# Kernel optimization log

Hardware: AMD Instinct MI355X
Metric: run time of the kernel (lower is better)

## Reference

```python
import jax, jax.numpy as jnp
import numpy as np

N, D = 16384, 128
T = 0.07


def setup_inputs() -> dict:
    key = jax.random.key(0)
    k1, k2 = jax.random.split(key)
    anchors = jax.random.normal(k1, (N, D), dtype=jnp.float32)
    positives = jax.random.normal(k2, (N, D), dtype=jnp.float32)
    return {"anchors": anchors, "positives": positives}


def reference(anchors, positives):
    # L2-normalize along feature dim (eps matches torch F.normalize default 1e-12)
    a = anchors / jnp.maximum(jnp.linalg.norm(anchors, axis=-1, keepdims=True), 1e-12)
    p = positives / jnp.maximum(jnp.linalg.norm(positives, axis=-1, keepdims=True), 1e-12)
    logits = (a @ p.T) / T  # [N, N]
    # cross-entropy with diagonal labels, mean reduction
    logz = jax.nn.logsumexp(logits, axis=-1)  # [N]
    diag = jnp.diagonal(logits)  # [N]
    return jnp.mean(logz - diag)
```

## Files before the change

### kernel.cpp

```cpp
#include <hip/hip_runtime.h>
#include <hip/hip_bf16.h>

#define N_ROWS 16384
#define DIM 128

constexpr float INV_T = 1.0f / 0.07f;
constexpr float LOG2E = 1.4426950408889634f;
constexpr float C1    = INV_T * LOG2E;
constexpr float SOP   = 4.5398160f;
constexpr float LN2   = 0.69314718055994530942f;

typedef int   v4i    __attribute__((ext_vector_type(4)));
typedef int   v8i    __attribute__((ext_vector_type(8)));
typedef float f32x16 __attribute__((ext_vector_type(16)));

typedef const __attribute__((address_space(1))) void* gptr1_t;
typedef __attribute__((address_space(3))) void*       sptr3_t;

#define TILE_BYTES 4096
#define BM 256
#define WROWS 64
#define COLSPLIT 16
#define COLS_PER (N_ROWS / COLSPLIT)
#define NJT (COLS_PER / 32)

__global__ __launch_bounds__(256) void norm_kernel(
    const float* __restrict__ A, const float* __restrict__ P,
    ushort* __restrict__ a8u, ushort* __restrict__ p8u,
    float* __restrict__ diag, float* __restrict__ sacc)
{
    if (threadIdx.x < 4) sacc[blockIdx.x * 4 + threadIdx.x] = 0.f;
    int row  = blockIdx.x * 4 + (threadIdx.x >> 6);
    int lane = threadIdx.x & 63;
    float2 av = *(const float2*)(A + (size_t)row * DIM + lane * 2);
    float2 pv = *(const float2*)(P + (size_t)row * DIM + lane * 2);
    float ssa = av.x * av.x + av.y * av.y;
    float ssp = pv.x * pv.x + pv.y * pv.y;
    float dp  = av.x * pv.x + av.y * pv.y;
    #pragma unroll
    for (int m = 1; m < 64; m <<= 1) {
        ssa += __shfl_xor(ssa, m);
        ssp += __shfl_xor(ssp, m);
        dp  += __shfl_xor(dp,  m);
    }
    float ra = 1.0f / fmaxf(sqrtf(ssa), 1e-12f);
    float rp = 1.0f / fmaxf(sqrtf(ssp), 1e-12f);
    if (lane == 0) diag[row] = dp * ra * rp * INV_T;
    float sa = ra * SOP, sp = rp * SOP;
    int apk = __builtin_amdgcn_cvt_pk_fp8_f32(av.x * sa, av.y * sa, 0, false);
    int ppk = __builtin_amdgcn_cvt_pk_fp8_f32(pv.x * sp, pv.y * sp, 0, false);
    a8u[(size_t)row * 64 + lane] = (ushort)apk;
    size_t off = (size_t)(row >> 5) * 2048 + (lane >> 5) * 1024
               + ((lane >> 4) & 1) * 512 + ((lane >> 3) & 1) * 256
               + (row & 31) * 8 + (lane & 7);
    p8u[off] = (ushort)ppk;
}

__global__ __launch_bounds__(256, 2) void lse_kernel(
    const ushort* __restrict__ a8u, const ushort* __restrict__ p8u,
    float* __restrict__ s_accum)
{
    __shared__ __attribute__((aligned(16))) char btile[3][TILE_BYTES];

    int colseg = blockIdx.x & (COLSPLIT - 1);
    int rowblk = blockIdx.x / COLSPLIT;
    int wave = threadIdx.x >> 6;
    int lane = threadIdx.x & 63;
    int c31  = lane & 31, hi = lane >> 5;
    int row0 = rowblk * BM + wave * WROWS;

    const char* a8 = (const char*)a8u;
    v8i afA0 = *(const v8i*)(a8 + (size_t)(row0 + c31) * 128 +       hi * 32);
    v8i afA1 = *(const v8i*)(a8 + (size_t)(row0 + c31) * 128 + 64  + hi * 32);
    v8i afB0 = *(const v8i*)(a8 + (size_t)(row0 + 32 + c31) * 128 +      hi * 32);
    v8i afB1 = *(const v8i*)(a8 + (size_t)(row0 + 32 + c31) * 128 + 64 + hi * 32);

    f32x16 cinit;
    #pragma unroll
    for (int r = 0; r < 16; ++r) cinit[r] = -C1;

    float s0[16], s1[16];
    #pragma unroll
    for (int r = 0; r < 16; ++r) { s0[r] = 0.f; s1[r] = 0.f; }

    const char* seg = (const char*)p8u + (size_t)colseg * NJT * TILE_BYTES;
    char* lds = (char*)&btile[0][0];
    int choff = wave * 1024 + lane * 16;

    auto STAGE = [&](int t, int buf) {
        __builtin_amdgcn_global_load_lds(
            (gptr1_t)(seg + (size_t)t * TILE_BYTES + choff),
            (sptr3_t)(lds + buf * TILE_BYTES + choff), 16, 0, 0);
    };

    int rdoff = hi * 1024 + c31 * 16;

    f32x16 acc0, acc1;

    STAGE(0, 0);
    STAGE(1, 1);

    for (int jt = 0; jt < NJT; ++jt) {
        if (jt < NJT - 1) asm volatile("s_waitcnt vmcnt(1)" ::: "memory");
        else              asm volatile("s_waitcnt vmcnt(0)" ::: "memory");
        __builtin_amdgcn_s_barrier();
        __builtin_amdgcn_sched_barrier(0);

        if (jt + 2 < NJT) STAGE(jt + 2, (jt + 2) % 3);

        const char* tb = lds + (jt % 3) * TILE_BYTES;
        v4i x0 = *(const v4i*)(tb + rdoff);
        v4i y0 = *(const v4i*)(tb + rdoff + 512);
        v4i x1 = *(const v4i*)(tb + 2048 + rdoff);
        v4i y1 = *(const v4i*)(tb + 2048 + rdoff + 512);
        v8i b0, b1;
        #pragma unroll
        for (int j = 0; j < 4; ++j) {
            b0[j] = x0[j]; b0[4 + j] = y0[j];
            b1[j] = x1[j]; b1[4 + j] = y1[j];
        }

        __builtin_amdgcn_s_setprio(1);
        acc0 = __builtin_amdgcn_mfma_scale_f32_32x32x64_f8f6f4(
            afA0, b0, cinit, 0, 0, 0, 0x7f7f7f7f, 0, 0x7f7f7f7f);
        acc1 = __builtin_amdgcn_mfma_scale_f32_32x32x64_f8f6f4(
            afB0, b0, cinit, 0, 0, 0, 0x7f7f7f7f, 0, 0x7f7f7f7f);
        acc0 = __builtin_amdgcn_mfma_scale_f32_32x32x64_f8f6f4(
            afA1, b1, acc0, 0, 0, 0, 0x7f7f7f7f, 0, 0x7f7f7f7f);
        acc1 = __builtin_amdgcn_mfma_scale_f32_32x32x64_f8f6f4(
            afB1, b1, acc1, 0, 0, 0, 0x7f7f7f7f, 0, 0x7f7f7f7f);
        __builtin_amdgcn_s_setprio(0);

        #pragma unroll
        for (int r = 0; r < 16; ++r) {
            s0[r] += __builtin_amdgcn_exp2f(acc0[r]);
            s1[r] += __builtin_amdgcn_exp2f(acc1[r]);
        }
    }

    #pragma unroll
    for (int t = 0; t < 2; ++t)
        #pragma unroll
        for (int r = 0; r < 16; ++r) {
            float v = (t ? s1[r] : s0[r]);
            v += __shfl_xor(v, 1);
            v += __shfl_xor(v, 2);
            v += __shfl_xor(v, 4);
            v += __shfl_xor(v, 8);
            v += __shfl_xor(v, 16);
            if (c31 == 0)
                atomicAdd(&s_accum[row0 + t * 32 + (r & 3) + 8 * (r >> 2) + 4 * hi], v);
        }
}

__global__ __launch_bounds__(1024) void finalize_kernel(
    const float* __restrict__ s_acc, const float* __restrict__ diag,
    float* __restrict__ out)
{
    float acc = 0.f;
    int t = threadIdx.x;
    #pragma unroll
    for (int i = 0; i < 4; ++i) {
        int idx = (i * 1024 + t) * 4;
        float4 sv = *(const float4*)(s_acc + idx);
        float4 dv = *(const float4*)(diag + idx);
        acc += __builtin_amdgcn_logf(sv.x) * LN2 + INV_T - dv.x;
        acc += __builtin_amdgcn_logf(sv.y) * LN2 + INV_T - dv.y;
        acc += __builtin_amdgcn_logf(sv.z) * LN2 + INV_T - dv.z;
        acc += __builtin_amdgcn_logf(sv.w) * LN2 + INV_T - dv.w;
    }
    #pragma unroll
    for (int m = 1; m < 64; m <<= 1) acc += __shfl_xor(acc, m);
    __shared__ float wsum[16];
    if ((t & 63) == 0) wsum[t >> 6] = acc;
    __syncthreads();
    if (t == 0) {
        float r = 0.f;
        #pragma unroll
        for (int i = 0; i < 16; ++i) r += wsum[i];
        out[0] = r / (float)N_ROWS;
    }
}

extern "C" void kernel_launch(void* const* d_in, const int* in_sizes, int n_in,
                              void* d_out, int out_size, void* d_ws, size_t ws_size,
                              hipStream_t stream)
{
    const float* A = (const float*)d_in[0];
    const float* P = (const float*)d_in[1];
    float* out = (float*)d_out;

    char* ws = (char*)d_ws;
    ushort* a8u  = (ushort*)ws;
    ushort* p8u  = (ushort*)(ws + (size_t)2 * 1024 * 1024);
    float*  diag = (float*)(ws + (size_t)4 * 1024 * 1024);
    float*  sacc = (float*)(ws + (size_t)4 * 1024 * 1024 + 65536);

    norm_kernel<<<N_ROWS / 4, 256, 0, stream>>>(A, P, a8u, p8u, diag, sacc);
    lse_kernel<<<(N_ROWS / BM) * COLSPLIT, 256, 0, stream>>>(a8u, p8u, sacc);
    finalize_kernel<<<1, 1024, 0, stream>>>(sacc, diag, out);
}
```

Before: 62.85 us.

## Use single-wave blocks with private double-buffered B tiles, dropping barriers

The LSE kernel moves from 256-thread blocks, where four waves share a triple-buffered B tile, to 64-thread single-wave blocks. Each wave now stages the whole 4KB tile itself with four global_load_lds calls into a double buffer. The next prefetch is issued only after the LDS reads finish (lgkmcnt(0)), so no s_barrier is needed. This removes the cross-wave barrier stalls, but each B tile is now fetched four times as often from global/L2 and blocks are smaller, which changes occupancy and scheduling.

```diff
diff --git a/kernel.cpp b/kernel.cpp
--- a/kernel.cpp
+++ b/kernel.cpp
@@ -18,7 +18,6 @@
 typedef __attribute__((address_space(3))) void*       sptr3_t;
 
 #define TILE_BYTES 4096
-#define BM 256
 #define WROWS 64
 #define COLSPLIT 16
 #define COLS_PER (N_ROWS / COLSPLIT)
@@ -56,18 +55,17 @@
     p8u[off] = (ushort)ppk;
 }
 
-__global__ __launch_bounds__(256, 2) void lse_kernel(
+__global__ __launch_bounds__(64) void lse_kernel(
     const ushort* __restrict__ a8u, const ushort* __restrict__ p8u,
     float* __restrict__ s_accum)
 {
-    __shared__ __attribute__((aligned(16))) char btile[3][TILE_BYTES];
+    __shared__ __attribute__((aligned(16))) char btile[2][TILE_BYTES];
 
     int colseg = blockIdx.x & (COLSPLIT - 1);
-    int rowblk = blockIdx.x / COLSPLIT;
-    int wave = threadIdx.x >> 6;
-    int lane = threadIdx.x & 63;
+    int rowwav = blockIdx.x >> 4;
+    int lane = threadIdx.x;
     int c31  = lane & 31, hi = lane >> 5;
-    int row0 = rowblk * BM + wave * WROWS;
+    int row0 = rowwav * WROWS;
 
     const char* a8 = (const char*)a8u;
     v8i afA0 = *(const v8i*)(a8 + (size_t)(row0 + c31) * 128 +       hi * 32);
@@ -85,30 +83,27 @@
 
     const char* seg = (const char*)p8u + (size_t)colseg * NJT * TILE_BYTES;
     char* lds = (char*)&btile[0][0];
-    int choff = wave * 1024 + lane * 16;
+    int loff = lane * 16;
 
     auto STAGE = [&](int t, int buf) {
-        __builtin_amdgcn_global_load_lds(
-            (gptr1_t)(seg + (size_t)t * TILE_BYTES + choff),
-            (sptr3_t)(lds + buf * TILE_BYTES + choff), 16, 0, 0);
+        const char* src = seg + (size_t)t * TILE_BYTES + loff;
+        char* dst = lds + buf * TILE_BYTES + loff;
+        #pragma unroll
+        for (int i = 0; i < 4; ++i)
+            __builtin_amdgcn_global_load_lds(
+                (gptr1_t)(src + i * 1024), (sptr3_t)(dst + i * 1024), 16, 0, 0);
     };
 
     int rdoff = hi * 1024 + c31 * 16;
-
-    f32x16 acc0, acc1;
 
     STAGE(0, 0);
     STAGE(1, 1);
 
     for (int jt = 0; jt < NJT; ++jt) {
-        if (jt < NJT - 1) asm volatile("s_waitcnt vmcnt(1)" ::: "memory");
+        if (jt < NJT - 1) asm volatile("s_waitcnt vmcnt(4)" ::: "memory");
         else              asm volatile("s_waitcnt vmcnt(0)" ::: "memory");
-        __builtin_amdgcn_s_barrier();
-        __builtin_amdgcn_sched_barrier(0);
-
-        if (jt + 2 < NJT) STAGE(jt + 2, (jt + 2) % 3);
-
-        const char* tb = lds + (jt % 3) * TILE_BYTES;
+
+        const char* tb = lds + (jt & 1) * TILE_BYTES;
         v4i x0 = *(const v4i*)(tb + rdoff);
         v4i y0 = *(const v4i*)(tb + rdoff + 512);
         v4i x1 = *(const v4i*)(tb + 2048 + rdoff);
@@ -119,11 +114,15 @@
             b0[j] = x0[j]; b0[4 + j] = y0[j];
             b1[j] = x1[j]; b1[4 + j] = y1[j];
         }
+        asm volatile("s_waitcnt lgkmcnt(0)" ::: "memory");
+        __builtin_amdgcn_sched_barrier(0);
+
+        if (jt + 2 < NJT) STAGE(jt + 2, jt & 1);
 
         __builtin_amdgcn_s_setprio(1);
-        acc0 = __builtin_amdgcn_mfma_scale_f32_32x32x64_f8f6f4(
+        f32x16 acc0 = __builtin_amdgcn_mfma_scale_f32_32x32x64_f8f6f4(
             afA0, b0, cinit, 0, 0, 0, 0x7f7f7f7f, 0, 0x7f7f7f7f);
-        acc1 = __builtin_amdgcn_mfma_scale_f32_32x32x64_f8f6f4(
+        f32x16 acc1 = __builtin_amdgcn_mfma_scale_f32_32x32x64_f8f6f4(
             afB0, b0, cinit, 0, 0, 0, 0x7f7f7f7f, 0, 0x7f7f7f7f);
         acc0 = __builtin_amdgcn_mfma_scale_f32_32x32x64_f8f6f4(
             afA1, b1, acc0, 0, 0, 0, 0x7f7f7f7f, 0, 0x7f7f7f7f);
@@ -197,6 +196,6 @@
     float*  sacc = (float*)(ws + (size_t)4 * 1024 * 1024 + 65536);
 
     norm_kernel<<<N_ROWS / 4, 256, 0, stream>>>(A, P, a8u, p8u, diag, sacc);
-    lse_kernel<<<(N_ROWS / BM) * COLSPLIT, 256, 0, stream>>>(a8u, p8u, sacc);
+    lse_kernel<<<(N_ROWS / WROWS) * COLSPLIT, 64, 0, stream>>>(a8u, p8u, sacc);
     finalize_kernel<<<1, 1024, 0, stream>>>(sacc, diag, out);
 }
```

After: 70.71 us. 1.12x slower.

## Load B tiles directly into registers with double-buffered prefetch, dropping LDS staging

Applied to the files above, without the earlier changes.

Replaces the global_load_lds triple-buffered LDS staging and per-iteration workgroup barriers with direct global-to-register loads of the B fragments. Each wave double-buffers two tiles in registers (even/odd sets) and prefetches the next tile while running MFMA and exp2 on the current one. This removes the barrier and LDS round-trip cost per tile. In exchange, each wave fetches the B tile itself from L2/global instead of sharing one LDS copy across the block, so global traffic per block goes up and more VGPRs are needed.

```diff
diff --git a/kernel.cpp b/kernel.cpp
--- a/kernel.cpp
+++ b/kernel.cpp
@@ -13,9 +13,6 @@
 typedef int   v4i    __attribute__((ext_vector_type(4)));
 typedef int   v8i    __attribute__((ext_vector_type(8)));
 typedef float f32x16 __attribute__((ext_vector_type(16)));
-
-typedef const __attribute__((address_space(1))) void* gptr1_t;
-typedef __attribute__((address_space(3))) void*       sptr3_t;
 
 #define TILE_BYTES 4096
 #define BM 256
@@ -60,8 +57,6 @@
     const ushort* __restrict__ a8u, const ushort* __restrict__ p8u,
     float* __restrict__ s_accum)
 {
-    __shared__ __attribute__((aligned(16))) char btile[3][TILE_BYTES];
-
     int colseg = blockIdx.x & (COLSPLIT - 1);
     int rowblk = blockIdx.x / COLSPLIT;
     int wave = threadIdx.x >> 6;
@@ -83,60 +78,55 @@
     #pragma unroll
     for (int r = 0; r < 16; ++r) { s0[r] = 0.f; s1[r] = 0.f; }
 
-    const char* seg = (const char*)p8u + (size_t)colseg * NJT * TILE_BYTES;
-    char* lds = (char*)&btile[0][0];
-    int choff = wave * 1024 + lane * 16;
+    const char* base = (const char*)p8u
+                     + (size_t)colseg * NJT * TILE_BYTES + hi * 1024 + c31 * 16;
 
-    auto STAGE = [&](int t, int buf) {
-        __builtin_amdgcn_global_load_lds(
-            (gptr1_t)(seg + (size_t)t * TILE_BYTES + choff),
-            (sptr3_t)(lds + buf * TILE_BYTES + choff), 16, 0, 0);
-    };
+    v4i eX0, eY0, eX1, eY1;
+    v4i oX0, oY0, oX1, oY1;
 
-    int rdoff = hi * 1024 + c31 * 16;
+#define LOADSET_E(t) { const char* tb = base + (size_t)(t) * TILE_BYTES;      \
+        eX0 = *(const v4i*)(tb);        eY0 = *(const v4i*)(tb + 512);        \
+        eX1 = *(const v4i*)(tb + 2048); eY1 = *(const v4i*)(tb + 2560); }
+#define LOADSET_O(t) { const char* tb = base + (size_t)(t) * TILE_BYTES;      \
+        oX0 = *(const v4i*)(tb);        oY0 = *(const v4i*)(tb + 512);        \
+        oX1 = *(const v4i*)(tb + 2048); oY1 = *(const v4i*)(tb + 2560); }
 
-    f32x16 acc0, acc1;
+#define COMPUTE(X0, Y0, X1, Y1) {                                             \
+        v8i b0 = __builtin_shufflevector(X0, Y0, 0, 1, 2, 3, 4, 5, 6, 7);     \
+        v8i b1 = __builtin_shufflevector(X1, Y1, 0, 1, 2, 3, 4, 5, 6, 7);     \
+        __builtin_amdgcn_s_setprio(1);                                        \
+        f32x16 acc0 = __builtin_amdgcn_mfma_scale_f32_32x32x64_f8f6f4(        \
+            afA0, b0, cinit, 0, 0, 0, 0x7f7f7f7f, 0, 0x7f7f7f7f);             \
+        f32x16 acc1 = __builtin_amdgcn_mfma_scale_f32_32x32x64_f8f6f4(        \
+            afB0, b0, cinit, 0, 0, 0, 0x7f7f7f7f, 0, 0x7f7f7f7f);             \
+        acc0 = __builtin_amdgcn_mfma_scale_f32_32x32x64_f8f6f4(               \
+            afA1, b1, acc0, 0, 0, 0, 0x7f7f7f7f, 0, 0x7f7f7f7f);              \
+        acc1 = __builtin_amdgcn_mfma_scale_f32_32x32x64_f8f6f4(               \
+            afB1, b1, acc1, 0, 0, 0, 0x7f7f7f7f, 0, 0x7f7f7f7f);              \
+        __builtin_amdgcn_s_setprio(0);                                        \
+        _Pragma("unroll")                                                     \
+        for (int r = 0; r < 16; ++r) {                                        \
+            s0[r] += __builtin_amdgcn_exp2f(acc0[r]);                         \
+            s1[r] += __builtin_amdgcn_exp2f(acc1[r]);                         \
+        } }
 
-    STAGE(0, 0);
-    STAGE(1, 1);
+    LOADSET_E(0);
+    LOADSET_O(1);
 
-    for (int jt = 0; jt < NJT; ++jt) {
-        if (jt < NJT - 1) asm volatile("s_waitcnt vmcnt(1)" ::: "memory");
-        else              asm volatile("s_waitcnt vmcnt(0)" ::: "memory");
-        __builtin_amdgcn_s_barrier();
-        __builtin_amdgcn_sched_barrier(0);
+    for (int m = 0; m < 15; ++m) {
+        v4i x0 = eX0, y0 = eY0, x1 = eX1, y1 = eY1;
+        LOADSET_E(2 * m + 2);
+        COMPUTE(x0, y0, x1, y1);
+        v4i u0 = oX0, v0 = oY0, u1 = oX1, v1 = oY1;
+        LOADSET_O(2 * m + 3);
+        COMPUTE(u0, v0, u1, v1);
+    }
+    COMPUTE(eX0, eY0, eX1, eY1);
+    COMPUTE(oX0, oY0, oX1, oY1);
 
-        if (jt + 2 < NJT) STAGE(jt + 2, (jt + 2) % 3);
-
-        const char* tb = lds + (jt % 3) * TILE_BYTES;
-        v4i x0 = *(const v4i*)(tb + rdoff);
-        v4i y0 = *(const v4i*)(tb + rdoff + 512);
-        v4i x1 = *(const v4i*)(tb + 2048 + rdoff);
-        v4i y1 = *(const v4i*)(tb + 2048 + rdoff + 512);
-        v8i b0, b1;
-        #pragma unroll
-        for (int j = 0; j < 4; ++j) {
-            b0[j] = x0[j]; b0[4 + j] = y0[j];
-            b1[j] = x1[j]; b1[4 + j] = y1[j];
-        }
-
-        __builtin_amdgcn_s_setprio(1);
-        acc0 = __builtin_amdgcn_mfma_scale_f32_32x32x64_f8f6f4(
-            afA0, b0, cinit, 0, 0, 0, 0x7f7f7f7f, 0, 0x7f7f7f7f);
-        acc1 = __builtin_amdgcn_mfma_scale_f32_32x32x64_f8f6f4(
-            afB0, b0, cinit, 0, 0, 0, 0x7f7f7f7f, 0, 0x7f7f7f7f);
-        acc0 = __builtin_amdgcn_mfma_scale_f32_32x32x64_f8f6f4(
-            afA1, b1, acc0, 0, 0, 0, 0x7f7f7f7f, 0, 0x7f7f7f7f);
-        acc1 = __builtin_amdgcn_mfma_scale_f32_32x32x64_f8f6f4(
-            afB1, b1, acc1, 0, 0, 0, 0x7f7f7f7f, 0, 0x7f7f7f7f);
-        __builtin_amdgcn_s_setprio(0);
-
-        #pragma unroll
-        for (int r = 0; r < 16; ++r) {
-            s0[r] += __builtin_amdgcn_exp2f(acc0[r]);
-            s1[r] += __builtin_amdgcn_exp2f(acc1[r]);
-        }
-    }
+#undef LOADSET_E
+#undef LOADSET_O
+#undef COMPUTE
 
     #pragma unroll
     for (int t = 0; t < 2; ++t)
```

Measured after the change: 63.77 us. About the same (+1.5%).

## Halve rows per wave in LSE kernel to one 32-row MFMA tile

Applied to the files above, without the earlier changes.

Each wave now handles 32 anchor rows instead of 64, so the block tile drops from 256 to 128 rows and the grid doubles. Every B tile staged into LDS is therefore used by half as many MFMAs, which doubles the total B traffic and the global-to-LDS staging. In exchange each wave holds fewer registers and more waves can be resident. The exp2 work per wave halves, which may help the exp-bound loop hide latency, but per-block load overhead and atomic count per row stay the same while block count grows.

```diff
diff --git a/kernel.cpp b/kernel.cpp
--- a/kernel.cpp
+++ b/kernel.cpp
@@ -18,8 +18,8 @@
 typedef __attribute__((address_space(3))) void*       sptr3_t;
 
 #define TILE_BYTES 4096
-#define BM 256
-#define WROWS 64
+#define BM 128
+#define WROWS 32
 #define COLSPLIT 16
 #define COLS_PER (N_ROWS / COLSPLIT)
 #define NJT (COLS_PER / 32)
@@ -70,18 +70,12 @@
     int row0 = rowblk * BM + wave * WROWS;
 
     const char* a8 = (const char*)a8u;
-    v8i afA0 = *(const v8i*)(a8 + (size_t)(row0 + c31) * 128 +       hi * 32);
-    v8i afA1 = *(const v8i*)(a8 + (size_t)(row0 + c31) * 128 + 64  + hi * 32);
-    v8i afB0 = *(const v8i*)(a8 + (size_t)(row0 + 32 + c31) * 128 +      hi * 32);
-    v8i afB1 = *(const v8i*)(a8 + (size_t)(row0 + 32 + c31) * 128 + 64 + hi * 32);
+    v8i afA0 = *(const v8i*)(a8 + (size_t)(row0 + c31) * 128 +      hi * 32);
+    v8i afA1 = *(const v8i*)(a8 + (size_t)(row0 + c31) * 128 + 64 + hi * 32);
 
-    f32x16 cinit;
+    float s0[16];
     #pragma unroll
-    for (int r = 0; r < 16; ++r) cinit[r] = -C1;
-
-    float s0[16], s1[16];
-    #pragma unroll
-    for (int r = 0; r < 16; ++r) { s0[r] = 0.f; s1[r] = 0.f; }
+    for (int r = 0; r < 16; ++r) s0[r] = 0.f;
 
     const char* seg = (const char*)p8u + (size_t)colseg * NJT * TILE_BYTES;
     char* lds = (char*)&btile[0][0];
@@ -94,8 +88,6 @@
     };
 
     int rdoff = hi * 1024 + c31 * 16;
-
-    f32x16 acc0, acc1;
 
     STAGE(0, 0);
     STAGE(1, 1);
@@ -120,37 +112,33 @@
             b1[j] = x1[j]; b1[4 + j] = y1[j];
         }
 
+        f32x16 acc;
+        #pragma unroll
+        for (int r = 0; r < 16; ++r) acc[r] = -C1;
+
         __builtin_amdgcn_s_setprio(1);
-        acc0 = __builtin_amdgcn_mfma_scale_f32_32x32x64_f8f6f4(
-            afA0, b0, cinit, 0, 0, 0, 0x7f7f7f7f, 0, 0x7f7f7f7f);
-        acc1 = __builtin_amdgcn_mfma_scale_f32_32x32x64_f8f6f4(
-            afB0, b0, cinit, 0, 0, 0, 0x7f7f7f7f, 0, 0x7f7f7f7f);
-        acc0 = __builtin_amdgcn_mfma_scale_f32_32x32x64_f8f6f4(
-            afA1, b1, acc0, 0, 0, 0, 0x7f7f7f7f, 0, 0x7f7f7f7f);
-        acc1 = __builtin_amdgcn_mfma_scale_f32_32x32x64_f8f6f4(
-            afB1, b1, acc1, 0, 0, 0, 0x7f7f7f7f, 0, 0x7f7f7f7f);
+        acc = __builtin_amdgcn_mfma_scale_f32_32x32x64_f8f6f4(
+            afA0, b0, acc, 0, 0, 0, 0x7f7f7f7f, 0, 0x7f7f7f7f);
+        acc = __builtin_amdgcn_mfma_scale_f32_32x32x64_f8f6f4(
+            afA1, b1, acc, 0, 0, 0, 0x7f7f7f7f, 0, 0x7f7f7f7f);
         __builtin_amdgcn_s_setprio(0);
 
         #pragma unroll
-        for (int r = 0; r < 16; ++r) {
-            s0[r] += __builtin_amdgcn_exp2f(acc0[r]);
-            s1[r] += __builtin_amdgcn_exp2f(acc1[r]);
-        }
+        for (int r = 0; r < 16; ++r)
+            s0[r] += __builtin_amdgcn_exp2f(acc[r]);
     }
 
     #pragma unroll
-    for (int t = 0; t < 2; ++t)
-        #pragma unroll
-        for (int r = 0; r < 16; ++r) {
-            float v = (t ? s1[r] : s0[r]);
-            v += __shfl_xor(v, 1);
-            v += __shfl_xor(v, 2);
-            v += __shfl_xor(v, 4);
-            v += __shfl_xor(v, 8);
-            v += __shfl_xor(v, 16);
-            if (c31 == 0)
-                atomicAdd(&s_accum[row0 + t * 32 + (r & 3) + 8 * (r >> 2) + 4 * hi], v);
-        }
+    for (int r = 0; r < 16; ++r) {
+        float v = s0[r];
+        v += __shfl_xor(v, 1);
+        v += __shfl_xor(v, 2);
+        v += __shfl_xor(v, 4);
+        v += __shfl_xor(v, 8);
+        v += __shfl_xor(v, 16);
+        if (c31 == 0)
+            atomicAdd(&s_accum[row0 + (r & 3) + 8 * (r >> 2) + 4 * hi], v);
+    }
 }
 
 __global__ __launch_bounds__(1024) void finalize_kernel(
```

After: 61.04 us. 1.03x faster.
